# Optimization experiments

Hardware: AMD Instinct MI355X
Metric: run time of the kernel (lower is better)

The kernel has to match this reference:

```python
import jax, jax.numpy as jnp
import numpy as np

B, P, D = 8, 196, 768       # batch, patches per image, hidden
H, DH = 12, 64              # heads, head dim (H*DH == D)
L = 4                       # GAT layers
THRESH = 0.1                # GraphGenerator similarity threshold
SLOPE = 0.2                 # LeakyReLU negative slope (DGL GATConv default)
NEG = -1e9


def setup_inputs() -> dict:
    key = jax.random.key(0)
    k0, k1, k2, k3, k4 = jax.random.split(key, 5)
    l_feat = jax.random.normal(k0, (B, P, D), jnp.float32)
    r_feat = jax.random.normal(k1, (B, P, D), jnp.float32)
    W = jax.random.normal(k2, (L, D, H * DH), jnp.float32) / np.float32(np.sqrt(D))
    a_src = jax.random.normal(k3, (L, H, DH), jnp.float32) / np.float32(np.sqrt(DH))
    a_dst = jax.random.normal(k4, (L, H, DH), jnp.float32) / np.float32(np.sqrt(DH))
    b = jnp.zeros((L, H * DH), jnp.float32)
    return dict(l_feat=l_feat, r_feat=r_feat, W=W, a_src=a_src, a_dst=a_dst, b=b)


def _leaky(x):
    return jax.nn.leaky_relu(x, SLOPE)


def _gat_layer_bipartite(h, Wl, a_s, a_d, bias, mask_rl, Nl):
    # Graph: edges l->r where mask_rl[r, l] is True, plus a self loop on every node.
    # l-nodes therefore only see themselves (alpha = 1).
    N = h.shape[0]
    z = (h @ Wl).reshape(N, H, DH)                      # [N, H, DH]
    el = jnp.einsum('nhd,hd->nh', z, a_s)               # src score
    er = jnp.einsum('nhd,hd->nh', z, a_d)               # dst score
    zl, zr = z[:Nl], z[Nl:]
    cross = _leaky(el[:Nl][None, :, :] + er[Nl:][:, None, :])   # [Nr, Nl, H]
    cross = jnp.where(mask_rl[..., None], cross, NEG)
    self_r = _leaky(el[Nl:] + er[Nl:])                   # [Nr, H] self-loop logit
    logits = jnp.concatenate([cross, self_r[:, None, :]], axis=1)  # [Nr, Nl+1, H]
    alpha = jax.nn.softmax(logits, axis=1)
    out_r = jnp.einsum('rlh,lhd->rhd', alpha[:, :Nl], zl) + alpha[:, Nl][..., None] * zr
    out = jnp.concatenate([zl, out_r], axis=0)           # l-nodes: identity (self loop)
    return out.reshape(N, H * DH) + bias


def _gat_layer_pool(h, Wl, a_s, a_d, bias):
    # Graph from _gather: every node -> first node of its P-block (col = img_node
    # repeat_interleave) plus add_self_loop. The root's self edge thus appears TWICE,
    # giving it multiplicity 2 in the edge softmax. Non-root nodes: self loop only.
    N = h.shape[0]
    G = N // P
    z = (h @ Wl).reshape(G, P, H, DH)
    el = jnp.einsum('gphd,hd->gph', z, a_s)
    er = jnp.einsum('gphd,hd->gph', z, a_d)
    logits = _leaky(el + er[:, :1, :])                   # [G, P, H], dst = node 0
    logc = jnp.log(jnp.where(jnp.arange(P) == 0, 2.0, 1.0)).astype(h.dtype)
    alpha = jax.nn.softmax(logits + logc[None, :, None], axis=1)
    pooled = jnp.einsum('gph,gphd->ghd', alpha, z)       # root aggregation
    out = z.at[:, 0].set(pooled)                         # others keep self value
    return out.reshape(N, H * DH) + bias


def _gat(h, W, a_src, a_dst, b, layer_fn):
    for i in range(L):
        h = layer_fn(h, W[i], a_src[i], a_dst[i], b[i])
        if i < L - 1:
            h = jax.nn.elu(h)
    return h


def reference(l_feat, r_feat, W, a_src, a_dst, b):
    node_l = l_feat.reshape(-1, D)
    node_r = r_feat.reshape(-1, D)
    Nl = node_l.shape[0]
    # GraphGenerator: cosine-similarity threshold graph (edges l -> r)
    nl = node_l / jnp.linalg.norm(node_l, axis=-1, keepdims=True)
    nr = node_r / jnp.linalg.norm(node_r, axis=-1, keepdims=True)
    mask_rl = (nr @ nl.T) > THRESH                       # [Nr, Nl]
    h = jnp.concatenate([node_l, node_r], axis=0)        # [2*B*P, D]
    h = _gat(h, W, a_src, a_dst, b,
             lambda x, w, s, d, bb: _gat_layer_bipartite(x, w, s, d, bb, mask_rl, Nl))
    # second GAT pass on the pooling graph, then index_select the per-image roots
    h = _gat(h, W, a_src, a_dst, b, _gat_layer_pool)
    img = h[::P]                                         # img_node = arange(0, N, P)
    return img[:B], img[B:]                              # (node_feat_l, node_feat_r)
```

## Files before the change

### kernel.cpp

```cpp
#include <hip/hip_runtime.h>
#include <math.h>

#define NL    1568
#define NTOT  3136
#define DD    768
#define NH    12
#define DHD   64
#define WPR   49
#define MAXDEG 64
#define NKSTEP 24
#define LOG2F_ 0.69314718055994530942f

typedef _Float16 h8 __attribute__((ext_vector_type(8)));
typedef float f32x4 __attribute__((ext_vector_type(4)));
typedef float f32x16 __attribute__((ext_vector_type(16)));
#define MFMA16(a, b, c) __builtin_amdgcn_mfma_f32_16x16x32_f16(a, b, c, 0, 0, 0)
#define MFMA32(a, b, c) __builtin_amdgcn_mfma_f32_32x32x16_f16(a, b, c, 0, 0, 0)

__device__ __forceinline__ float leaky(float x) { return x > 0.f ? x : 0.2f * x; }

__device__ __forceinline__ void gld16(const _Float16* g, _Float16* l) {
  __builtin_amdgcn_global_load_lds(
      (const __attribute__((address_space(1))) void*)g,
      (__attribute__((address_space(3))) void*)l, 16, 0, 0);
}

__global__ __launch_bounds__(192) void conv_init(const float* __restrict__ lf, const float* __restrict__ rf,
                                                 _Float16* __restrict__ hi, _Float16* __restrict__ lo,
                                                 float* __restrict__ norms) {
  int n = blockIdx.x;
  int t = threadIdx.x;
  const float* src = (n < NL) ? lf + (size_t)n * DD : rf + (size_t)(n - NL) * DD;
  float4 v = reinterpret_cast<const float4*>(src)[t];
  _Float16 a0 = (_Float16)v.x, a1 = (_Float16)v.y, a2 = (_Float16)v.z, a3 = (_Float16)v.w;
  typedef _Float16 h4v __attribute__((ext_vector_type(4)));
  h4v hv = {a0, a1, a2, a3};
  h4v lv = {(_Float16)((v.x - (float)a0) * 2048.f), (_Float16)((v.y - (float)a1) * 2048.f),
            (_Float16)((v.z - (float)a2) * 2048.f), (_Float16)((v.w - (float)a3) * 2048.f)};
  size_t idx = (size_t)n * (DD / 4) + t;
  reinterpret_cast<h4v*>(hi)[idx] = hv;
  reinterpret_cast<h4v*>(lo)[idx] = lv;
  float s = v.x * v.x + v.y * v.y + v.z * v.z + v.w * v.w;
  #pragma unroll
  for (int o = 32; o; o >>= 1) s += __shfl_xor(s, o);
  __shared__ float red[3];
  if ((t & 63) == 0) red[t >> 6] = s;
  __syncthreads();
  if (t == 0) norms[n] = sqrtf(red[0] + red[1] + red[2]);
}

__global__ __launch_bounds__(256) void transp_W(const float* __restrict__ W, _Float16* __restrict__ Wthi) {
  __shared__ float tile[32][33];
  int kt = blockIdx.x * 32, nt = blockIdx.y * 32, i = blockIdx.z;
  int tx = threadIdx.x & 31, ty = threadIdx.x >> 5;
  const float* Wp = W + ((size_t)i * DD + kt) * DD + nt;
  #pragma unroll
  for (int p = 0; p < 4; ++p) tile[ty + p * 8][tx] = Wp[(size_t)(ty + p * 8) * DD + tx];
  __syncthreads();
  _Float16* oh = Wthi + ((size_t)i * DD + nt) * DD + kt;
  #pragma unroll
  for (int p = 0; p < 4; ++p) {
    int nn = ty + p * 8;
    oh[(size_t)nn * DD + tx] = (_Float16)tile[tx][nn];
  }
}

__global__ __launch_bounds__(256) void gemm_mfma(const _Float16* __restrict__ Ahi,
                                                 const _Float16* __restrict__ Bhi,
                                                 const float* __restrict__ a_s, const float* __restrict__ a_d,
                                                 const float* __restrict__ bias,
                                                 _Float16* __restrict__ zh,
                                                 float* __restrict__ el, float* __restrict__ er,
                                                 _Float16* __restrict__ ohhi,
                                                 int do_elu, int mode) {
  __shared__ _Float16 smA[2][2048];
  __shared__ _Float16 smB[2][4096];
  int t = threadIdx.x;
  int xcd = blockIdx.x & 7, pos = blockIdx.x >> 3;
  int orig = (xcd < 6 ? xcd * 37 : 222 + (xcd - 6) * 36) + pos;
  int bx = orig / 6, by = orig % 6;
  int m0 = bx * 64, n0 = by * 128;

  int rl = t >> 2;
  int kq_src = (t & 3) ^ ((rl >> 1) & 3);
  const _Float16* pA  = Ahi + (size_t)(m0 + rl) * DD + kq_src * 8;
  const _Float16* pB1 = Bhi + (size_t)(n0 + rl) * DD + kq_src * 8;
  const _Float16* pB2 = Bhi + (size_t)(n0 + 64 + rl) * DD + kq_src * 8;
  int w = t >> 6, l = t & 63;
  int chA  = w * 512;
  int chB2 = 2048 + w * 512;

  int cl = l & 31, hi = l >> 5;
  int rw = (w >> 1) * 32, cw = (w & 1) * 64;
  int arow = rw + cl;
  int aOff0 = arow * 32 + ((hi)     ^ ((arow >> 1) & 3)) * 8;
  int aOff1 = arow * 32 + ((hi + 2) ^ ((arow >> 1) & 3)) * 8;
  int brow0 = cw + cl, brow1 = cw + 32 + cl;
  int bOff00 = brow0 * 32 + ((hi)     ^ ((brow0 >> 1) & 3)) * 8;
  int bOff01 = brow0 * 32 + ((hi + 2) ^ ((brow0 >> 1) & 3)) * 8;
  int bOff10 = brow1 * 32 + ((hi)     ^ ((brow1 >> 1) & 3)) * 8;
  int bOff11 = brow1 * 32 + ((hi + 2) ^ ((brow1 >> 1) & 3)) * 8;

  f32x16 acc0, acc1;
  #pragma unroll
  for (int i = 0; i < 16; ++i) { acc0[i] = 0.f; acc1[i] = 0.f; }

  gld16(pA,  &smA[0][chA]);
  gld16(pB1, &smB[0][chA]);
  gld16(pB2, &smB[0][chB2]);
  __syncthreads();

  for (int step = 0; step < NKSTEP; ++step) {
    int buf = step & 1;
    if (step < NKSTEP - 1) {
      int kb = (step + 1) * 32;
      gld16(pA + kb,  &smA[buf ^ 1][chA]);
      gld16(pB1 + kb, &smB[buf ^ 1][chA]);
      gld16(pB2 + kb, &smB[buf ^ 1][chB2]);
    }
    h8 a0  = *reinterpret_cast<const h8*>(&smA[buf][aOff0]);
    h8 a1  = *reinterpret_cast<const h8*>(&smA[buf][aOff1]);
    h8 b00 = *reinterpret_cast<const h8*>(&smB[buf][bOff00]);
    h8 b01 = *reinterpret_cast<const h8*>(&smB[buf][bOff01]);
    h8 b10 = *reinterpret_cast<const h8*>(&smB[buf][bOff10]);
    h8 b11 = *reinterpret_cast<const h8*>(&smB[buf][bOff11]);
    acc0 = MFMA32(a0, b00, acc0);
    acc1 = MFMA32(a0, b10, acc1);
    acc0 = MFMA32(a1, b01, acc0);
    acc1 = MFMA32(a1, b11, acc1);
    __syncthreads();
  }

  int hd = by * 2 + (w & 1);
  float as0 = a_s[hd * DHD + cl],      ad0 = a_d[hd * DHD + cl];
  float as1 = a_s[hd * DHD + 32 + cl], ad1 = a_d[hd * DHD + 32 + cl];
  int c0 = n0 + cw + cl, c1 = c0 + 32;
  float bv0 = bias[c0], bv1 = bias[c1];
  #pragma unroll
  for (int r = 0; r < 16; ++r) {
    int row = m0 + rw + (r & 3) + 8 * (r >> 2) + 4 * hi;
    float z0 = acc0[r], z1 = acc1[r];
    zh[(size_t)row * DD + c0] = (_Float16)z0;
    zh[(size_t)row * DD + c1] = (_Float16)z1;
    bool wh = (mode == 0) ? (row < NL) : (row % 196 != 0);
    if (wh) {
      float o0 = z0 + bv0, o1 = z1 + bv1;
      if (do_elu) {
        o0 = o0 > 0.f ? o0 : expm1f(o0);
        o1 = o1 > 0.f ? o1 : expm1f(o1);
      }
      ohhi[(size_t)row * DD + c0] = (_Float16)o0;
      ohhi[(size_t)row * DD + c1] = (_Float16)o1;
    }
    float s1 = z0 * as0 + z1 * as1;
    float s2 = z0 * ad0 + z1 * ad1;
    #pragma unroll
    for (int o = 1; o < 32; o <<= 1) {
      s1 += __shfl_xor(s1, o);
      s2 += __shfl_xor(s2, o);
    }
    if (cl == 0) {
      el[(size_t)row * NH + hd] = s1;
      er[(size_t)row * NH + hd] = s2;
    }
  }
}

__global__ __launch_bounds__(256) void mask_mfma(const _Float16* __restrict__ Hhi, const _Float16* __restrict__ Hlo,
                                                 const float* __restrict__ norms, unsigned* __restrict__ mask) {
  __shared__ _Float16 sm[2][4][2048];
  __shared__ unsigned mw[64][2];
  int t = threadIdx.x;
  int r0 = blockIdx.x * 64, l0 = blockIdx.y * 64;

  int rl = t >> 2;
  int kq_src = (t & 3) ^ ((t >> 3) & 3);
  int ra = r0 + rl; if (ra >= NL) ra = NL - 1;
  int la = l0 + rl; if (la >= NL) la = NL - 1;
  size_t aoff = (size_t)(NL + ra) * DD + kq_src * 8;
  size_t boff = (size_t)la * DD + kq_src * 8;
  const _Float16* pAhi = Hhi + aoff;
  const _Float16* pAlo = Hlo + aoff;
  const _Float16* pBhi = Hhi + boff;
  const _Float16* pBlo = Hlo + boff;
  int ch = (t >> 6) * 512;

  int ln = t & 63, wv = t >> 6;
  int fr = ln & 15, kg = ln >> 4;
  int kq8 = (kg ^ ((fr >> 1) & 3)) * 8;
  int aRead = (wv * 16 + fr) * 32 + kq8;

  f32x4 zero = {0.f, 0.f, 0.f, 0.f};
  f32x4 acc1[4], acc2[4];
  #pragma unroll
  for (int cg = 0; cg < 4; ++cg) { acc1[cg] = zero; acc2[cg] = zero; }
  if (t < 128) mw[t >> 1][t & 1] = 0u;

  gld16(pAhi, &sm[0][0][ch]);
  gld16(pAlo, &sm[0][1][ch]);
  gld16(pBhi, &sm[0][2][ch]);
  gld16(pBlo, &sm[0][3][ch]);
  __syncthreads();

  for (int step = 0; step < NKSTEP; ++step) {
    int buf = step & 1;
    if (step < NKSTEP - 1) {
      int kb = (step + 1) * 32;
      gld16(pAhi + kb, &sm[buf ^ 1][0][ch]);
      gld16(pAlo + kb, &sm[buf ^ 1][1][ch]);
      gld16(pBhi + kb, &sm[buf ^ 1][2][ch]);
      gld16(pBlo + kb, &sm[buf ^ 1][3][ch]);
    }
    h8 ah = *reinterpret_cast<const h8*>(&sm[buf][0][aRead]);
    h8 al = *reinterpret_cast<const h8*>(&sm[buf][1][aRead]);
    #pragma unroll
    for (int cg = 0; cg < 4; ++cg) {
      int bRead = (cg * 16 + fr) * 32 + kq8;
      h8 bh = *reinterpret_cast<const h8*>(&sm[buf][2][bRead]);
      h8 bl = *reinterpret_cast<const h8*>(&sm[buf][3][bRead]);
      acc1[cg] = MFMA16(ah, bh, acc1[cg]);
      acc2[cg] = MFMA16(ah, bl, acc2[cg]);
      acc2[cg] = MFMA16(al, bh, acc2[cg]);
    }
    __syncthreads();
  }

  int rloc = wv * 16 + kg * 4;
  float nrv[4];
  #pragma unroll
  for (int i = 0; i < 4; ++i) {
    int r = r0 + rloc + i;
    nrv[i] = norms[NL + (r < NL ? r : NL - 1)];
  }
  #pragma unroll
  for (int cg = 0; cg < 4; ++cg) {
    int lloc = cg * 16 + fr;
    int l = l0 + lloc;
    float nlv = norms[l < NL ? l : NL - 1];
    #pragma unroll
    for (int i = 0; i < 4; ++i) {
      int r = r0 + rloc + i;
      float dot = acc1[cg][i] + acc2[cg][i] * (1.f / 2048.f);
      if (r < NL && l < NL && dot > 0.1f * nrv[i] * nlv)
        atomicOr(&mw[rloc + i][lloc >> 5], 1u << (lloc & 31));
    }
  }
  __syncthreads();
  if (t < 128) {
    int rr = t >> 1, w = t & 1;
    int rg = r0 + rr, wg = blockIdx.y * 2 + w;
    if (rg < NL && wg < WPR) mask[(size_t)rg * WPR + wg] = mw[rr][w];
  }
}

__global__ __launch_bounds__(64) void build_csr(const unsigned* __restrict__ mask,
                                                int* __restrict__ nbr, int* __restrict__ deg) {
  int r = blockIdx.x * 64 + threadIdx.x;
  if (r >= NL) return;
  const unsigned* mr = mask + (size_t)r * WPR;
  int* out = nbr + (size_t)r * MAXDEG;
  int cnt = 0;
  #pragma unroll 7
  for (int w = 0; w < WPR; ++w) {
    unsigned m = mr[w];
    while (m) {
      int bpos = __ffs(m) - 1;
      m &= m - 1;
      if (cnt < MAXDEG) out[cnt] = w * 32 + bpos;
      ++cnt;
    }
  }
  deg[r] = cnt < MAXDEG ? cnt : MAXDEG;
}

__global__ __launch_bounds__(768) void bip_fused(const _Float16* __restrict__ zh, const float* __restrict__ el,
                                                 const float* __restrict__ er, const int* __restrict__ nbr,
                                                 const int* __restrict__ deg, const float* __restrict__ bias,
                                                 _Float16* __restrict__ ohhi,
                                                 int do_elu) {
  int r = blockIdx.x;
  int R = NL + r;
  int t = threadIdx.x;
  int dg = deg[r];
  __shared__ int nb_s[MAXDEG];
  __shared__ float wbuf[MAXDEG * NH];
  __shared__ float den_s[NH], wself_s[NH];
  if (t < dg) nb_s[t] = nbr[(size_t)r * MAXDEG + t];
  __syncthreads();
  if (t < dg * NH) {
    int j = t / NH, h2 = t - j * NH;
    wbuf[t] = el[(size_t)nb_s[j] * NH + h2];
  }
  __syncthreads();
  if (t < NH) {
    float er_r = er[(size_t)R * NH + t];
    float s = leaky(el[(size_t)R * NH + t] + er_r);
    float mx = s;
    for (int j = 0; j < dg; ++j) mx = fmaxf(mx, leaky(wbuf[j * NH + t] + er_r));
    float den = 0.f;
    for (int j = 0; j < dg; ++j) {
      float w = expf(leaky(wbuf[j * NH + t] + er_r) - mx);
      wbuf[j * NH + t] = w;
      den += w;
    }
    float ws = expf(s - mx);
    den_s[t] = den + ws;
    wself_s[t] = ws;
  }
  __syncthreads();
  int h2 = t >> 6;
  float acc = wself_s[h2] * (float)zh[(size_t)R * DD + t];
  for (int j = 0; j < dg; ++j)
    acc = fmaf(wbuf[j * NH + h2], (float)zh[(size_t)nb_s[j] * DD + t], acc);
  float o = acc / den_s[h2] + bias[t];
  if (do_elu) o = o > 0.f ? o : expm1f(o);
  ohhi[(size_t)R * DD + t] = (_Float16)o;
}

__global__ __launch_bounds__(256) void pool_attn2(const _Float16* __restrict__ zh, const float* __restrict__ el,
                                                  const float* __restrict__ er, const float* __restrict__ bias,
                                                  _Float16* __restrict__ ohhi,
                                                  float* __restrict__ root_out, int do_elu) {
  int g = blockIdx.x, h = blockIdx.y;
  int base = g * 196;
  int t = threadIdx.x;
  int w = t >> 6, d = t & 63;
  __shared__ float wb[196];
  __shared__ float red[4];
  __shared__ float accP[4][64];
  float er0 = er[(size_t)base * NH + h];
  float lg = -INFINITY;
  if (t < 196) {
    lg = leaky(el[(size_t)(base + t) * NH + h] + er0);
    if (t == 0) lg += LOG2F_;
  }
  float m = lg;
  #pragma unroll
  for (int o = 32; o; o >>= 1) m = fmaxf(m, __shfl_xor(m, o));
  if ((t & 63) == 0) red[w] = m;
  __syncthreads();
  float mx = fmaxf(fmaxf(red[0], red[1]), fmaxf(red[2], red[3]));
  float wgt = (t < 196) ? expf(lg - mx) : 0.f;
  if (t < 196) wb[t] = wgt;
  float dn = wgt;
  #pragma unroll
  for (int o = 32; o; o >>= 1) dn += __shfl_xor(dn, o);
  __syncthreads();
  if ((t & 63) == 0) red[w] = dn;
  __syncthreads();
  float den = red[0] + red[1] + red[2] + red[3];
  float acc = 0.f;
  int p0 = w * 49;
  #pragma unroll 7
  for (int p = p0; p < p0 + 49; ++p)
    acc = fmaf(wb[p], (float)zh[(size_t)(base + p) * DD + h * DHD + d], acc);
  accP[w][d] = acc;
  __syncthreads();
  if (w == 0) {
    float o = (accP[0][d] + accP[1][d] + accP[2][d] + accP[3][d]) / den + bias[h * DHD + d];
    if (do_elu) o = o > 0.f ? o : expm1f(o);
    int c = h * DHD + d;
    ohhi[(size_t)base * DD + c] = (_Float16)o;
    root_out[(size_t)g * DD + c] = o;
  }
}

extern "C" void kernel_launch(void* const* d_in, const int* in_sizes, int n_in,
                              void* d_out, int out_size, void* d_ws, size_t ws_size,
                              hipStream_t stream) {
  const float* l_feat = (const float*)d_in[0];
  const float* r_feat = (const float*)d_in[1];
  const float* W      = (const float*)d_in[2];
  const float* a_src  = (const float*)d_in[3];
  const float* a_dst  = (const float*)d_in[4];
  const float* b      = (const float*)d_in[5];
  float* out = (float*)d_out;

  float* el    = (float*)d_ws;
  float* er    = el + (size_t)NTOT * NH;
  float* norms = er + (size_t)NTOT * NH;
  float* hroot = norms + NTOT;
  unsigned* mask = (unsigned*)(hroot + 16 * DD);
  int* nbr = (int*)(mask + (size_t)NL * WPR);
  int* deg = nbr + (size_t)NL * MAXDEG;
  _Float16* hhiA = (_Float16*)(deg + NL);
  _Float16* hloA = hhiA + (size_t)NTOT * DD;
  _Float16* hhiB = hloA + (size_t)NTOT * DD;
  _Float16* Wthi = hhiB + (size_t)NTOT * DD;
  _Float16* zh   = Wthi + (size_t)4 * DD * DD;

  _Float16* hhi[2] = {hhiA, hhiB};

  conv_init<<<NTOT, 192, 0, stream>>>(l_feat, r_feat, hhiA, hloA, norms);
  transp_W<<<dim3(24, 24, 4), 256, 0, stream>>>(W, Wthi);
  mask_mfma<<<dim3(25, 25), 256, 0, stream>>>(hhiA, hloA, norms, mask);
  build_csr<<<(NL + 63) / 64, 64, 0, stream>>>(mask, nbr, deg);

  for (int i = 0; i < 4; ++i) {
    const float* bi = b + (size_t)i * DD;
    int do_elu = (i < 3) ? 1 : 0;
    int ib = i & 1, ob = (i + 1) & 1;
    gemm_mfma<<<294, 256, 0, stream>>>(hhi[ib],
        Wthi + (size_t)i * DD * DD,
        a_src + (size_t)i * NH * DHD, a_dst + (size_t)i * NH * DHD,
        bi, zh, el, er, hhi[ob], do_elu, 0);
    bip_fused<<<NL, 768, 0, stream>>>(zh, el, er, nbr, deg, bi, hhi[ob], do_elu);
  }

  for (int i = 0; i < 4; ++i) {
    const float* bi = b + (size_t)i * DD;
    int do_elu = (i < 3) ? 1 : 0;
    int L = 4 + i;
    int ib = L & 1, ob = (L + 1) & 1;
    gemm_mfma<<<294, 256, 0, stream>>>(hhi[ib],
        Wthi + (size_t)i * DD * DD,
        a_src + (size_t)i * NH * DHD, a_dst + (size_t)i * NH * DHD,
        bi, zh, el, er, hhi[ob], do_elu, 1);
    pool_attn2<<<dim3(16, NH), 256, 0, stream>>>(zh, el, er, bi, hhi[ob],
        (i == 3) ? out : hroot, do_elu);
  }
}
```

Before: 308.2 us.

## Halve GEMM M-tile to 32 rows, doubling block count for better CU occupancy

The z = h·W GEMM tile changes from 64x128 to 32x128, so the grid grows from 294 to 588 blocks. On a 256-CU part this fills the machine more evenly. Each wave now owns a single 32x32 accumulator, and the per-head el/er partial dot products are combined across wave pairs through shared memory. The XCD remapping is updated for the new block count. In exchange, W traffic per output row doubles and each block does less MFMA work per LDS load.

```diff
diff --git a/kernel.cpp b/kernel.cpp
--- a/kernel.cpp
+++ b/kernel.cpp
@@ -73,96 +73,93 @@
                                                  float* __restrict__ el, float* __restrict__ er,
                                                  _Float16* __restrict__ ohhi,
                                                  int do_elu, int mode) {
-  __shared__ _Float16 smA[2][2048];
+  __shared__ _Float16 smA[2][1024];
   __shared__ _Float16 smB[2][4096];
+  __shared__ float elp[4][2][16], erp[4][2][16];
   int t = threadIdx.x;
   int xcd = blockIdx.x & 7, pos = blockIdx.x >> 3;
-  int orig = (xcd < 6 ? xcd * 37 : 222 + (xcd - 6) * 36) + pos;
+  int orig = (xcd < 4 ? xcd * 74 : 296 + (xcd - 4) * 73) + pos;
   int bx = orig / 6, by = orig % 6;
-  int m0 = bx * 64, n0 = by * 128;
-
-  int rl = t >> 2;
-  int kq_src = (t & 3) ^ ((rl >> 1) & 3);
-  const _Float16* pA  = Ahi + (size_t)(m0 + rl) * DD + kq_src * 8;
-  const _Float16* pB1 = Bhi + (size_t)(n0 + rl) * DD + kq_src * 8;
-  const _Float16* pB2 = Bhi + (size_t)(n0 + 64 + rl) * DD + kq_src * 8;
+  int m0 = bx * 32, n0 = by * 128;
+
   int w = t >> 6, l = t & 63;
+  int rlA = t >> 2;
+  int kqA = (t & 3) ^ ((rlA >> 1) & 3);
+  const _Float16* pA = Ahi + (size_t)(m0 + (rlA & 31)) * DD + kqA * 8;
+  int rlB0 = t >> 2, rlB1 = 64 + rlB0;
+  int kqB0 = (t & 3) ^ ((rlB0 >> 1) & 3);
+  int kqB1 = (t & 3) ^ ((rlB1 >> 1) & 3);
+  const _Float16* pB0 = Bhi + (size_t)(n0 + rlB0) * DD + kqB0 * 8;
+  const _Float16* pB1 = Bhi + (size_t)(n0 + rlB1) * DD + kqB1 * 8;
   int chA  = w * 512;
-  int chB2 = 2048 + w * 512;
+  int chB0 = w * 512;
+  int chB1 = 2048 + w * 512;
 
   int cl = l & 31, hi = l >> 5;
-  int rw = (w >> 1) * 32, cw = (w & 1) * 64;
-  int arow = rw + cl;
-  int aOff0 = arow * 32 + ((hi)     ^ ((arow >> 1) & 3)) * 8;
-  int aOff1 = arow * 32 + ((hi + 2) ^ ((arow >> 1) & 3)) * 8;
-  int brow0 = cw + cl, brow1 = cw + 32 + cl;
-  int bOff00 = brow0 * 32 + ((hi)     ^ ((brow0 >> 1) & 3)) * 8;
-  int bOff01 = brow0 * 32 + ((hi + 2) ^ ((brow0 >> 1) & 3)) * 8;
-  int bOff10 = brow1 * 32 + ((hi)     ^ ((brow1 >> 1) & 3)) * 8;
-  int bOff11 = brow1 * 32 + ((hi + 2) ^ ((brow1 >> 1) & 3)) * 8;
-
-  f32x16 acc0, acc1;
-  #pragma unroll
-  for (int i = 0; i < 16; ++i) { acc0[i] = 0.f; acc1[i] = 0.f; }
-
-  gld16(pA,  &smA[0][chA]);
-  gld16(pB1, &smB[0][chA]);
-  gld16(pB2, &smB[0][chB2]);
+  int cw = w * 32;
+  int aOff0 = cl * 32 + ((hi)     ^ ((cl >> 1) & 3)) * 8;
+  int aOff1 = cl * 32 + ((hi + 2) ^ ((cl >> 1) & 3)) * 8;
+  int brow = cw + cl;
+  int bOff0 = brow * 32 + ((hi)     ^ ((brow >> 1) & 3)) * 8;
+  int bOff1 = brow * 32 + ((hi + 2) ^ ((brow >> 1) & 3)) * 8;
+
+  f32x16 acc;
+  #pragma unroll
+  for (int i = 0; i < 16; ++i) acc[i] = 0.f;
+
+  if (t < 128) gld16(pA, &smA[0][chA]);
+  gld16(pB0, &smB[0][chB0]);
+  gld16(pB1, &smB[0][chB1]);
   __syncthreads();
 
   for (int step = 0; step < NKSTEP; ++step) {
     int buf = step & 1;
     if (step < NKSTEP - 1) {
       int kb = (step + 1) * 32;
-      gld16(pA + kb,  &smA[buf ^ 1][chA]);
-      gld16(pB1 + kb, &smB[buf ^ 1][chA]);
-      gld16(pB2 + kb, &smB[buf ^ 1][chB2]);
-    }
-    h8 a0  = *reinterpret_cast<const h8*>(&smA[buf][aOff0]);
-    h8 a1  = *reinterpret_cast<const h8*>(&smA[buf][aOff1]);
-    h8 b00 = *reinterpret_cast<const h8*>(&smB[buf][bOff00]);
-    h8 b01 = *reinterpret_cast<const h8*>(&smB[buf][bOff01]);
-    h8 b10 = *reinterpret_cast<const h8*>(&smB[buf][bOff10]);
-    h8 b11 = *reinterpret_cast<const h8*>(&smB[buf][bOff11]);
-    acc0 = MFMA32(a0, b00, acc0);
-    acc1 = MFMA32(a0, b10, acc1);
-    acc0 = MFMA32(a1, b01, acc0);
-    acc1 = MFMA32(a1, b11, acc1);
+      if (t < 128) gld16(pA + kb, &smA[buf ^ 1][chA]);
+      gld16(pB0 + kb, &smB[buf ^ 1][chB0]);
+      gld16(pB1 + kb, &smB[buf ^ 1][chB1]);
+    }
+    h8 a0 = *reinterpret_cast<const h8*>(&smA[buf][aOff0]);
+    h8 a1 = *reinterpret_cast<const h8*>(&smA[buf][aOff1]);
+    h8 b0 = *reinterpret_cast<const h8*>(&smB[buf][bOff0]);
+    h8 b1 = *reinterpret_cast<const h8*>(&smB[buf][bOff1]);
+    acc = MFMA32(a0, b0, acc);
+    acc = MFMA32(a1, b1, acc);
     __syncthreads();
   }
 
-  int hd = by * 2 + (w & 1);
-  float as0 = a_s[hd * DHD + cl],      ad0 = a_d[hd * DHD + cl];
-  float as1 = a_s[hd * DHD + 32 + cl], ad1 = a_d[hd * DHD + 32 + cl];
-  int c0 = n0 + cw + cl, c1 = c0 + 32;
-  float bv0 = bias[c0], bv1 = bias[c1];
+  int hd = by * 2 + (w >> 1);
+  float asv = a_s[hd * DHD + (w & 1) * 32 + cl];
+  float adv = a_d[hd * DHD + (w & 1) * 32 + cl];
+  int c = n0 + cw + cl;
+  float bv = bias[c];
   #pragma unroll
   for (int r = 0; r < 16; ++r) {
-    int row = m0 + rw + (r & 3) + 8 * (r >> 2) + 4 * hi;
-    float z0 = acc0[r], z1 = acc1[r];
-    zh[(size_t)row * DD + c0] = (_Float16)z0;
-    zh[(size_t)row * DD + c1] = (_Float16)z1;
+    int row = m0 + (r & 3) + 8 * (r >> 2) + 4 * hi;
+    float z = acc[r];
+    zh[(size_t)row * DD + c] = (_Float16)z;
     bool wh = (mode == 0) ? (row < NL) : (row % 196 != 0);
     if (wh) {
-      float o0 = z0 + bv0, o1 = z1 + bv1;
-      if (do_elu) {
-        o0 = o0 > 0.f ? o0 : expm1f(o0);
-        o1 = o1 > 0.f ? o1 : expm1f(o1);
-      }
-      ohhi[(size_t)row * DD + c0] = (_Float16)o0;
-      ohhi[(size_t)row * DD + c1] = (_Float16)o1;
-    }
-    float s1 = z0 * as0 + z1 * as1;
-    float s2 = z0 * ad0 + z1 * ad1;
+      float o = z + bv;
+      if (do_elu) o = o > 0.f ? o : expm1f(o);
+      ohhi[(size_t)row * DD + c] = (_Float16)o;
+    }
+    float s1 = z * asv, s2 = z * adv;
     #pragma unroll
     for (int o = 1; o < 32; o <<= 1) {
       s1 += __shfl_xor(s1, o);
       s2 += __shfl_xor(s2, o);
     }
-    if (cl == 0) {
-      el[(size_t)row * NH + hd] = s1;
-      er[(size_t)row * NH + hd] = s2;
-    }
+    if (cl == 0) { elp[w][hi][r] = s1; erp[w][hi][r] = s2; }
+  }
+  __syncthreads();
+  if (t < 64) {
+    int hp = t >> 5, hi2 = (t >> 4) & 1, r2 = t & 15;
+    int row = m0 + (r2 & 3) + 8 * (r2 >> 2) + 4 * hi2;
+    int hd2 = by * 2 + hp;
+    el[(size_t)row * NH + hd2] = elp[2 * hp][hi2][r2] + elp[2 * hp + 1][hi2][r2];
+    er[(size_t)row * NH + hd2] = erp[2 * hp][hi2][r2] + erp[2 * hp + 1][hi2][r2];
   }
 }
 
@@ -400,7 +397,7 @@
     const float* bi = b + (size_t)i * DD;
     int do_elu = (i < 3) ? 1 : 0;
     int ib = i & 1, ob = (i + 1) & 1;
-    gemm_mfma<<<294, 256, 0, stream>>>(hhi[ib],
+    gemm_mfma<<<588, 256, 0, stream>>>(hhi[ib],
         Wthi + (size_t)i * DD * DD,
         a_src + (size_t)i * NH * DHD, a_dst + (size_t)i * NH * DHD,
         bi, zh, el, er, hhi[ob], do_elu, 0);
@@ -412,7 +409,7 @@
     int do_elu = (i < 3) ? 1 : 0;
     int L = 4 + i;
     int ib = L & 1, ob = (L + 1) & 1;
-    gemm_mfma<<<294, 256, 0, stream>>>(hhi[ib],
+    gemm_mfma<<<588, 256, 0, stream>>>(hhi[ib],
         Wthi + (size_t)i * DD * DD,
         a_src + (size_t)i * NH * DHD, a_dst + (size_t)i * NH * DHD,
         bi, zh, el, er, hhi[ob], do_elu, 1);
```

Measured after the change: 296.0 us. 4.0% less time.
